# Optimization experiments

Hardware: AMD Instinct MI355X
Metric: run time of the kernel (lower is better)

Reference implementation:

```python
import jax, jax.numpy as jnp
import numpy as np

N_EMB = 256
HEAD_SIZE = 64
B, S = 4, 4096


def setup_inputs() -> dict:
    key = jax.random.key(0)
    k1, k2, k3, k4 = jax.random.split(key, 4)
    return {
        "ini_emb": jax.random.normal(k1, (B, S, N_EMB), dtype=jnp.float32),
        "wk": jax.random.normal(k2, (N_EMB, HEAD_SIZE), dtype=jnp.float32) * (N_EMB ** -0.5),
        "wq": jax.random.normal(k3, (N_EMB, HEAD_SIZE), dtype=jnp.float32) * (N_EMB ** -0.5),
        "wv": jax.random.normal(k4, (N_EMB, HEAD_SIZE), dtype=jnp.float32) * (N_EMB ** -0.5),
    }


def reference(ini_emb, wk, wq, wv):
    # projections: [B,S,E] @ [E,H] -> [B,S,H]
    k = ini_emb @ wk
    q = ini_emb @ wq
    v = ini_emb @ wv
    # scores: [B,S,S]; NOTE: source scales by n_emb**-0.5, not head_size**-0.5
    scores = jnp.einsum("bqh,bkh->bqk", q, k) * (N_EMB ** -0.5)
    attn = jax.nn.softmax(scores, axis=-1)
    # output: [B,S,H]
    return jnp.einsum("bqk,bkh->bqh", attn, v)
```

## Files before the change

### kernel.cpp

```cpp
#include <hip/hip_runtime.h>


typedef short short4v __attribute__((ext_vector_type(4)));
typedef short short8v __attribute__((ext_vector_type(8)));
typedef float floatx4 __attribute__((ext_vector_type(4)));
typedef unsigned short u16;
typedef unsigned int u32;

#define SEQ 4096
#define EMB 256
#define HD 64
#define PADA 264
#define OSTR 68

static __device__ __forceinline__ u16 f2bf(float x) {
    union { float f; unsigned u; } v; v.f = x;
    unsigned r = v.u + 0x7FFFu + ((v.u >> 16) & 1u);
    return (u16)(r >> 16);
}

static __device__ __forceinline__ u32 cvt_pk_bf16(float a, float b) {
    u32 r;
    asm("v_cvt_pk_bf16_f32 %0, %1, %2" : "=v"(r) : "v"(a), "v"(b));
    return r;
}

static __device__ __forceinline__ short4v pack_bf4(float a, float b, float c, float d) {
    union { u32 u[2]; short4v s; } x;
    x.u[0] = cvt_pk_bf16(a, b);
    x.u[1] = cvt_pk_bf16(c, d);
    return x.s;
}

__global__ __launch_bounds__(256) void prep_w(
    const float* __restrict__ wk, const float* __restrict__ wq, const float* __restrict__ wv,
    u16* __restrict__ wt) {
    const int nt = blockIdx.x;
    const int t = threadIdx.x;
#pragma unroll
    for (int ss = 0; ss < 2; ++ss) {
        int slot = t + ss * 256;
        int kc = slot >> 6, lane = slot & 63;
        int ln15 = lane & 15, lq = lane >> 4;
        int cg = nt * 16 + ln15;
        int mat = cg >> 6, col = cg & 63;
        const float* W = (mat == 0) ? wq : (mat == 1) ? wk : wv;
        const float s = (mat == 0) ? 0.0625f * 1.44269504088896f : 1.0f;
        u32 w4[4];
#pragma unroll
        for (int p = 0; p < 2; ++p) {
#pragma unroll
            for (int d = 0; d < 2; ++d) {
                int e0 = kc * 32 + lq * 8 + p * 4 + d * 2;
                u16 lo = f2bf(W[(e0 + 0) * HD + col] * s);
                u16 hi = f2bf(W[(e0 + 1) * HD + col] * s);
                w4[p * 2 + d] = (u32)lo | ((u32)hi << 16);
            }
        }
        u32* dst = (u32*)wt + ((size_t)(nt * 8 + kc) * 64 + lane) * 4;
        *(uint4*)dst = make_uint4(w4[0], w4[1], w4[2], w4[3]);
    }
}

__global__ __launch_bounds__(256) void proj_mfma(
    const float* __restrict__ emb, const u16* __restrict__ wt,
    u16* __restrict__ qb, u16* __restrict__ kb, u16* __restrict__ vbt) {
    __shared__ u16 a_s[16 * PADA];
    const int t = threadIdx.x;
    const int lane = t & 63;
    const int wave = t >> 6;
    const int ln15 = lane & 15;
    const int lq = lane >> 4;
    const size_t row0 = (size_t)blockIdx.x * 16;

#pragma unroll
    for (int c = 0; c < 4; ++c) {
        int f = t + c * 256;
        int row = f >> 6, e4 = (f & 63) * 4;
        float4 v = *(const float4*)(emb + (row0 + row) * EMB + e4);
        u32 lo = cvt_pk_bf16(v.x, v.y);
        u32 hi = cvt_pk_bf16(v.z, v.w);
        *(uint2*)&a_s[row * PADA + e4] = make_uint2(lo, hi);
    }
    __syncthreads();

    floatx4 acc[3];
#pragma unroll
    for (int j = 0; j < 3; ++j) {
        floatx4 z = { 0.f, 0.f, 0.f, 0.f };
        acc[j] = z;
    }

#pragma unroll
    for (int kc = 0; kc < 8; ++kc) {
        short8v a = *(const short8v*)&a_s[ln15 * PADA + kc * 32 + lq * 8];
#pragma unroll
        for (int j = 0; j < 3; ++j) {
            short8v b = *(const short8v*)(wt + (((size_t)(wave * 3 + j) * 8 + kc) * 64 + lane) * 8);
            acc[j] = __builtin_amdgcn_mfma_f32_16x16x32_bf16(a, b, acc[j], 0, 0, 0);
        }
    }

#pragma unroll
    for (int j = 0; j < 3; ++j) {
        int cg = (wave * 3 + j) * 16 + ln15;
        int mat = cg >> 6, col = cg & 63;
        if (mat < 2) {
            u16* O = (mat == 0) ? qb : kb;
#pragma unroll
            for (int r = 0; r < 4; ++r)
                O[(row0 + lq * 4 + r) * HD + col] = f2bf(acc[j][r]);
        } else {
            u32 lo = cvt_pk_bf16(acc[j][0], acc[j][1]);
            u32 hi = cvt_pk_bf16(acc[j][2], acc[j][3]);
            size_t bidx = row0 >> 12;
            size_t sl = (row0 & 4095) + lq * 4;
            *(uint2*)&vbt[(bidx * 64 + col) * SEQ + sl] = make_uint2(lo, hi);
        }
    }
}


template <bool PF>
static __device__ __forceinline__ void attn_step(
    const int tt, const int split, const int wave, const int ln15, const int lq,
    const u16* __restrict__ kpb, const u16* __restrict__ vpb,
    const short8v (&qf)[4][2], const short8v k0c, const short8v k1c,
    short8v& k0n, short8v& k1n,
    floatx4 (&oacc)[4][4], float (&lacc)[4]) {
    const int kw = (split * 16 + tt) * 64 + wave * 16;

    short4v vf[4];
#pragma unroll
    for (int ht = 0; ht < 4; ++ht)
        vf[ht] = *(const short4v*)(vpb + (size_t)(ht * 16 + ln15) * SEQ + kw + lq * 4);

    if (PF) {
        const int kwn = kw + 64;
        k0n = *(const short8v*)(kpb + (size_t)(kwn + ln15) * HD + lq * 8);
        k1n = *(const short8v*)(kpb + (size_t)(kwn + ln15) * HD + 32 + lq * 8);
    }

    floatx4 s[4];
    __builtin_amdgcn_s_setprio(1);
#pragma unroll
    for (int nt = 0; nt < 4; ++nt) {
        floatx4 z = { 0.f, 0.f, 0.f, 0.f };
        s[nt] = __builtin_amdgcn_mfma_f32_16x16x32_bf16(k0c, qf[nt][0], z, 0, 0, 0);
        s[nt] = __builtin_amdgcn_mfma_f32_16x16x32_bf16(k1c, qf[nt][1], s[nt], 0, 0, 0);
    }
    __builtin_amdgcn_s_setprio(0);

    short4v pf[4];
#pragma unroll
    for (int nt = 0; nt < 4; ++nt) {
        float p0 = __builtin_amdgcn_exp2f(s[nt][0]);
        float p1 = __builtin_amdgcn_exp2f(s[nt][1]);
        float p2 = __builtin_amdgcn_exp2f(s[nt][2]);
        float p3 = __builtin_amdgcn_exp2f(s[nt][3]);
        lacc[nt] += (p0 + p1) + (p2 + p3);
        pf[nt] = pack_bf4(p0, p1, p2, p3);
    }

    __builtin_amdgcn_s_setprio(1);
#pragma unroll
    for (int ht = 0; ht < 4; ++ht)
#pragma unroll
        for (int nt = 0; nt < 4; ++nt)
            oacc[ht][nt] = __builtin_amdgcn_mfma_f32_16x16x16bf16_1k(
                vf[ht], pf[nt], oacc[ht][nt], 0, 0, 0);
    __builtin_amdgcn_s_setprio(0);
}

__global__ __launch_bounds__(256) void attn_kernel(
    const u16* __restrict__ qb, const u16* __restrict__ kb, const u16* __restrict__ vbt,
    float* __restrict__ po, float* __restrict__ pml) {
    __shared__ float ored[64 * OSTR];
    __shared__ float lred[4 * 64];

    const int t = threadIdx.x;
    const int lane = t & 63;
    const int wave = t >> 6;
    const int ln15 = lane & 15;
    const int lq = lane >> 4;

    const int part = blockIdx.x;
    const int b = part >> 8;
    const int qt = (part >> 2) & 63;
    const int split = part & 3;
    const int q0 = qt * 64;

    const u16* __restrict__ qpb = qb + ((size_t)b * SEQ + q0) * HD;
    const u16* __restrict__ kpb = kb + (size_t)b * SEQ * HD;
    const u16* __restrict__ vpb = vbt + (size_t)b * HD * SEQ;

    short8v qf[4][2];
#pragma unroll
    for (int nt = 0; nt < 4; ++nt)
#pragma unroll
        for (int h = 0; h < 2; ++h)
            qf[nt][h] = *(const short8v*)(qpb + (size_t)(nt * 16 + ln15) * HD + h * 32 + lq * 8);

    floatx4 oacc[4][4];
#pragma unroll
    for (int ht = 0; ht < 4; ++ht)
#pragma unroll
        for (int nt = 0; nt < 4; ++nt) {
            floatx4 z = { 0.f, 0.f, 0.f, 0.f };
            oacc[ht][nt] = z;
        }
    float lacc[4] = { 0.f, 0.f, 0.f, 0.f };

    short8v kA0, kA1, kB0, kB1;
    {
        const int kw0 = (split * 16) * 64 + wave * 16;
        kA0 = *(const short8v*)(kpb + (size_t)(kw0 + ln15) * HD + lq * 8);
        kA1 = *(const short8v*)(kpb + (size_t)(kw0 + ln15) * HD + 32 + lq * 8);
    }

#pragma unroll 1
    for (int tth = 0; tth < 8; ++tth) {
        attn_step<true>(2 * tth,     split, wave, ln15, lq, kpb, vpb, qf,
                        kA0, kA1, kB0, kB1, oacc, lacc);
        attn_step<true>(2 * tth + 1, split, wave, ln15, lq, kpb, vpb, qf,
                        kB0, kB1, kA0, kA1, oacc, lacc);
    }

#pragma unroll
    for (int nt = 0; nt < 4; ++nt) {
        lacc[nt] += __shfl_xor(lacc[nt], 16);
        lacc[nt] += __shfl_xor(lacc[nt], 32);
    }
    if (lq == 0) {
#pragma unroll
        for (int nt = 0; nt < 4; ++nt)
            lred[wave * 64 + nt * 16 + ln15] = lacc[nt];
    }

    for (int s4 = 0; s4 < 4; ++s4) {
        if (wave == s4) {
#pragma unroll
            for (int nt = 0; nt < 4; ++nt)
#pragma unroll
                for (int ht = 0; ht < 4; ++ht) {
                    int idx = (nt * 16 + ln15) * OSTR + ht * 16 + lq * 4;
                    if (s4 == 0) {
                        *(floatx4*)&ored[idx] = oacc[ht][nt];
                    } else {
                        floatx4 old = *(floatx4*)&ored[idx];
                        old += oacc[ht][nt];
                        *(floatx4*)&ored[idx] = old;
                    }
                }
        }
        __syncthreads();
    }

    float* __restrict__ pob = po + (size_t)part * 4096;
#pragma unroll
    for (int i = 0; i < 4; ++i) {
        int f4 = t + i * 256;
        int q = f4 >> 4, h4 = (f4 & 15) * 4;
        *(float4*)&pob[q * HD + h4] = *(float4*)&ored[q * OSTR + h4];
    }
    if (t < 64)
        pml[part * 64 + t] = lred[t] + lred[64 + t] + lred[128 + t] + lred[192 + t];
}

__global__ __launch_bounds__(256) void reduce_kernel(
    const float* __restrict__ po, const float* __restrict__ pml,
    float* __restrict__ out) {
    __shared__ float ls[64];
    const int t = threadIdx.x;
    const int part0 = blockIdx.x * 4;
    const int bq = blockIdx.x;

    if (t < 64)
        ls[t] = pml[(part0 + 0) * 64 + t] + pml[(part0 + 1) * 64 + t]
              + pml[(part0 + 2) * 64 + t] + pml[(part0 + 3) * 64 + t];
    __syncthreads();

    const float* __restrict__ p0 = po + (size_t)(part0 + 0) * 4096;
    const float* __restrict__ p1 = po + (size_t)(part0 + 1) * 4096;
    const float* __restrict__ p2 = po + (size_t)(part0 + 2) * 4096;
    const float* __restrict__ p3 = po + (size_t)(part0 + 3) * 4096;
    float* __restrict__ ob = out + (((size_t)(bq >> 6) * SEQ + (size_t)(bq & 63) * 64)) * HD;

#pragma unroll
    for (int i = 0; i < 4; ++i) {
        int f4 = t + i * 256;
        int f = f4 * 4;
        int q = f4 >> 4;
        float4 a = *(const float4*)&p0[f];
        float4 c = *(const float4*)&p1[f];
        float4 d = *(const float4*)&p2[f];
        float4 e = *(const float4*)&p3[f];
        float inv = 1.0f / ls[q];
        float4 r;
        r.x = (a.x + c.x + d.x + e.x) * inv;
        r.y = (a.y + c.y + d.y + e.y) * inv;
        r.z = (a.z + c.z + d.z + e.z) * inv;
        r.w = (a.w + c.w + d.w + e.w) * inv;
        *(float4*)&ob[f] = r;
    }
}

extern "C" void kernel_launch(void* const* d_in, const int* in_sizes, int n_in,
                              void* d_out, int out_size, void* d_ws, size_t ws_size,
                              hipStream_t stream) {
    const float* emb = (const float*)d_in[0];
    const float* wk  = (const float*)d_in[1];
    const float* wq  = (const float*)d_in[2];
    const float* wv  = (const float*)d_in[3];

    u16* qb  = (u16*)d_ws;
    u16* kb  = (u16*)((char*)d_ws + (size_t)2 * 1024 * 1024);
    u16* vbt = (u16*)((char*)d_ws + (size_t)4 * 1024 * 1024);
    u16* wt  = (u16*)((char*)d_ws + (size_t)6 * 1024 * 1024);
    float* po  = (float*)((char*)d_ws + (size_t)6 * 1024 * 1024 + 256 * 1024);
    float* pml = (float*)((char*)d_ws + (size_t)22 * 1024 * 1024 + 256 * 1024);
    float* out = (float*)d_out;

    prep_w<<<12, 256, 0, stream>>>(wk, wq, wv, wt);
    proj_mfma<<<1024, 256, 0, stream>>>(emb, wt, qb, kb, vbt);
    attn_kernel<<<1024, 256, 0, stream>>>(qb, kb, vbt, po, pml);
    reduce_kernel<<<256, 256, 0, stream>>>(po, pml, out);
}
```

Before: 136.4 us.

## Halve KV splits, prefetch V fragments, and swizzle block-to-part mapping

Cuts the key-split count from 4 to 2, so each attention block walks 32 key tiles instead of 16, and the grid shrinks to 512 blocks. V fragments are now double-buffered and prefetched one step ahead, like K, with the last step peeled so it skips the prefetch. Block indices are remapped with a stride-8 swizzle, likely to spread work across XCDs and L2. The reduce kernel sums two partials instead of four, which cuts partial-output traffic, at the cost of fewer blocks and less parallelism on a large GPU.

Measured after the change: 131.4 us. 1.04x faster.

```diff
diff --git a/kernel.cpp b/kernel.cpp
--- a/kernel.cpp
+++ b/kernel.cpp
@@ -125,18 +125,17 @@
 static __device__ __forceinline__ void attn_step(
     const int tt, const int split, const int wave, const int ln15, const int lq,
     const u16* __restrict__ kpb, const u16* __restrict__ vpb,
-    const short8v (&qf)[4][2], const short8v k0c, const short8v k1c,
-    short8v& k0n, short8v& k1n,
+    const short8v (&qf)[4][2],
+    const short8v k0c, const short8v k1c, const short4v (&vfc)[4],
+    short8v& k0n, short8v& k1n, short4v (&vfn)[4],
     floatx4 (&oacc)[4][4], float (&lacc)[4]) {
-    const int kw = (split * 16 + tt) * 64 + wave * 16;
-
-    short4v vf[4];
-#pragma unroll
-    for (int ht = 0; ht < 4; ++ht)
-        vf[ht] = *(const short4v*)(vpb + (size_t)(ht * 16 + ln15) * SEQ + kw + lq * 4);
+    const int kw = (split * 32 + tt) * 64 + wave * 16;
 
     if (PF) {
         const int kwn = kw + 64;
+#pragma unroll
+        for (int ht = 0; ht < 4; ++ht)
+            vfn[ht] = *(const short4v*)(vpb + (size_t)(ht * 16 + ln15) * SEQ + kwn + lq * 4);
         k0n = *(const short8v*)(kpb + (size_t)(kwn + ln15) * HD + lq * 8);
         k1n = *(const short8v*)(kpb + (size_t)(kwn + ln15) * HD + 32 + lq * 8);
     }
@@ -168,7 +167,7 @@
 #pragma unroll
         for (int nt = 0; nt < 4; ++nt)
             oacc[ht][nt] = __builtin_amdgcn_mfma_f32_16x16x16bf16_1k(
-                vf[ht], pf[nt], oacc[ht][nt], 0, 0, 0);
+                vfc[ht], pf[nt], oacc[ht][nt], 0, 0, 0);
     __builtin_amdgcn_s_setprio(0);
 }
 
@@ -184,10 +183,10 @@
     const int ln15 = lane & 15;
     const int lq = lane >> 4;
 
-    const int part = blockIdx.x;
-    const int b = part >> 8;
-    const int qt = (part >> 2) & 63;
-    const int split = part & 3;
+    const int part = ((blockIdx.x & 7) << 6) | (blockIdx.x >> 3);
+    const int b = part >> 7;
+    const int qt = (part >> 1) & 63;
+    const int split = part & 1;
     const int q0 = qt * 64;
 
     const u16* __restrict__ qpb = qb + ((size_t)b * SEQ + q0) * HD;
@@ -212,19 +211,27 @@
     float lacc[4] = { 0.f, 0.f, 0.f, 0.f };
 
     short8v kA0, kA1, kB0, kB1;
+    short4v vfA[4], vfB[4];
     {
-        const int kw0 = (split * 16) * 64 + wave * 16;
+        const int kw0 = (split * 32) * 64 + wave * 16;
         kA0 = *(const short8v*)(kpb + (size_t)(kw0 + ln15) * HD + lq * 8);
         kA1 = *(const short8v*)(kpb + (size_t)(kw0 + ln15) * HD + 32 + lq * 8);
+#pragma unroll
+        for (int ht = 0; ht < 4; ++ht)
+            vfA[ht] = *(const short4v*)(vpb + (size_t)(ht * 16 + ln15) * SEQ + kw0 + lq * 4);
     }
 
 #pragma unroll 1
-    for (int tth = 0; tth < 8; ++tth) {
+    for (int tth = 0; tth < 15; ++tth) {
         attn_step<true>(2 * tth,     split, wave, ln15, lq, kpb, vpb, qf,
-                        kA0, kA1, kB0, kB1, oacc, lacc);
+                        kA0, kA1, vfA, kB0, kB1, vfB, oacc, lacc);
         attn_step<true>(2 * tth + 1, split, wave, ln15, lq, kpb, vpb, qf,
-                        kB0, kB1, kA0, kA1, oacc, lacc);
-    }
+                        kB0, kB1, vfB, kA0, kA1, vfA, oacc, lacc);
+    }
+    attn_step<true >(30, split, wave, ln15, lq, kpb, vpb, qf,
+                     kA0, kA1, vfA, kB0, kB1, vfB, oacc, lacc);
+    attn_step<false>(31, split, wave, ln15, lq, kpb, vpb, qf,
+                     kB0, kB1, vfB, kA0, kA1, vfA, oacc, lacc);
 
 #pragma unroll
     for (int nt = 0; nt < 4; ++nt) {
@@ -272,18 +279,15 @@
     float* __restrict__ out) {
     __shared__ float ls[64];
     const int t = threadIdx.x;
-    const int part0 = blockIdx.x * 4;
+    const int part0 = blockIdx.x * 2;
     const int bq = blockIdx.x;
 
     if (t < 64)
-        ls[t] = pml[(part0 + 0) * 64 + t] + pml[(part0 + 1) * 64 + t]
-              + pml[(part0 + 2) * 64 + t] + pml[(part0 + 3) * 64 + t];
+        ls[t] = pml[(part0 + 0) * 64 + t] + pml[(part0 + 1) * 64 + t];
     __syncthreads();
 
     const float* __restrict__ p0 = po + (size_t)(part0 + 0) * 4096;
     const float* __restrict__ p1 = po + (size_t)(part0 + 1) * 4096;
-    const float* __restrict__ p2 = po + (size_t)(part0 + 2) * 4096;
-    const float* __restrict__ p3 = po + (size_t)(part0 + 3) * 4096;
     float* __restrict__ ob = out + (((size_t)(bq >> 6) * SEQ + (size_t)(bq & 63) * 64)) * HD;
 
 #pragma unroll
@@ -293,14 +297,12 @@
         int q = f4 >> 4;
         float4 a = *(const float4*)&p0[f];
         float4 c = *(const float4*)&p1[f];
-        float4 d = *(const float4*)&p2[f];
-        float4 e = *(const float4*)&p3[f];
         float inv = 1.0f / ls[q];
         float4 r;
-        r.x = (a.x + c.x + d.x + e.x) * inv;
-        r.y = (a.y + c.y + d.y + e.y) * inv;
-        r.z = (a.z + c.z + d.z + e.z) * inv;
-        r.w = (a.w + c.w + d.w + e.w) * inv;
+        r.x = (a.x + c.x) * inv;
+        r.y = (a.y + c.y) * inv;
+        r.z = (a.z + c.z) * inv;
+        r.w = (a.w + c.w) * inv;
         *(float4*)&ob[f] = r;
     }
 }
@@ -323,6 +325,6 @@
 
     prep_w<<<12, 256, 0, stream>>>(wk, wq, wv, wt);
     proj_mfma<<<1024, 256, 0, stream>>>(emb, wt, qb, kb, vbt);
-    attn_kernel<<<1024, 256, 0, stream>>>(qb, kb, vbt, po, pml);
+    attn_kernel<<<512, 256, 0, stream>>>(qb, kb, vbt, po, pml);
     reduce_kernel<<<256, 256, 0, stream>>>(po, pml, out);
 }
```

## Stage K/V tiles through swizzled LDS with double buffering; widen projection tiles

Applied to the files above, without the earlier changes.

Attention now loads each 64-key K and V tile cooperatively with coalesced 16-byte global loads into XOR-swizzled, double-buffered shared memory, prefetching the next tile into registers while computing the current one. Before, each wave fetched its own strided fragments straight from global memory. Blocks are also remapped so consecutive block IDs spread across batch and query tiles. Separately, the projection kernel handles 32 rows per block so each weight fragment is reused for two MFMAs. This adds barriers and LDS traffic per tile and halves the number of projection blocks.

New measurement: 119.5 us. 12.4% less time.

```diff
diff --git a/kernel.cpp b/kernel.cpp
--- a/kernel.cpp
+++ b/kernel.cpp
@@ -65,16 +65,16 @@
 __global__ __launch_bounds__(256) void proj_mfma(
     const float* __restrict__ emb, const u16* __restrict__ wt,
     u16* __restrict__ qb, u16* __restrict__ kb, u16* __restrict__ vbt) {
-    __shared__ u16 a_s[16 * PADA];
+    __shared__ u16 a_s[32 * PADA];
     const int t = threadIdx.x;
     const int lane = t & 63;
     const int wave = t >> 6;
     const int ln15 = lane & 15;
     const int lq = lane >> 4;
-    const size_t row0 = (size_t)blockIdx.x * 16;
-
-#pragma unroll
-    for (int c = 0; c < 4; ++c) {
+    const size_t row0 = (size_t)blockIdx.x * 32;
+
+#pragma unroll
+    for (int c = 0; c < 8; ++c) {
         int f = t + c * 256;
         int row = f >> 6, e4 = (f & 63) * 4;
         float4 v = *(const float4*)(emb + (row0 + row) * EMB + e4);
@@ -84,70 +84,73 @@
     }
     __syncthreads();
 
-    floatx4 acc[3];
-#pragma unroll
-    for (int j = 0; j < 3; ++j) {
-        floatx4 z = { 0.f, 0.f, 0.f, 0.f };
-        acc[j] = z;
-    }
+    floatx4 acc[2][3];
+#pragma unroll
+    for (int rg = 0; rg < 2; ++rg)
+#pragma unroll
+        for (int j = 0; j < 3; ++j) {
+            floatx4 z = { 0.f, 0.f, 0.f, 0.f };
+            acc[rg][j] = z;
+        }
 
 #pragma unroll
     for (int kc = 0; kc < 8; ++kc) {
-        short8v a = *(const short8v*)&a_s[ln15 * PADA + kc * 32 + lq * 8];
+        short8v a0 = *(const short8v*)&a_s[ln15 * PADA + kc * 32 + lq * 8];
+        short8v a1 = *(const short8v*)&a_s[(16 + ln15) * PADA + kc * 32 + lq * 8];
 #pragma unroll
         for (int j = 0; j < 3; ++j) {
             short8v b = *(const short8v*)(wt + (((size_t)(wave * 3 + j) * 8 + kc) * 64 + lane) * 8);
-            acc[j] = __builtin_amdgcn_mfma_f32_16x16x32_bf16(a, b, acc[j], 0, 0, 0);
-        }
-    }
-
-#pragma unroll
-    for (int j = 0; j < 3; ++j) {
-        int cg = (wave * 3 + j) * 16 + ln15;
-        int mat = cg >> 6, col = cg & 63;
-        if (mat < 2) {
-            u16* O = (mat == 0) ? qb : kb;
-#pragma unroll
-            for (int r = 0; r < 4; ++r)
-                O[(row0 + lq * 4 + r) * HD + col] = f2bf(acc[j][r]);
-        } else {
-            u32 lo = cvt_pk_bf16(acc[j][0], acc[j][1]);
-            u32 hi = cvt_pk_bf16(acc[j][2], acc[j][3]);
-            size_t bidx = row0 >> 12;
-            size_t sl = (row0 & 4095) + lq * 4;
-            *(uint2*)&vbt[(bidx * 64 + col) * SEQ + sl] = make_uint2(lo, hi);
-        }
-    }
-}
-
-
-template <bool PF>
-static __device__ __forceinline__ void attn_step(
-    const int tt, const int split, const int wave, const int ln15, const int lq,
-    const u16* __restrict__ kpb, const u16* __restrict__ vpb,
-    const short8v (&qf)[4][2], const short8v k0c, const short8v k1c,
-    short8v& k0n, short8v& k1n,
-    floatx4 (&oacc)[4][4], float (&lacc)[4]) {
-    const int kw = (split * 16 + tt) * 64 + wave * 16;
-
+            acc[0][j] = __builtin_amdgcn_mfma_f32_16x16x32_bf16(a0, b, acc[0][j], 0, 0, 0);
+            acc[1][j] = __builtin_amdgcn_mfma_f32_16x16x32_bf16(a1, b, acc[1][j], 0, 0, 0);
+        }
+    }
+
+#pragma unroll
+    for (int rg = 0; rg < 2; ++rg) {
+        const size_t row0g = row0 + rg * 16;
+#pragma unroll
+        for (int j = 0; j < 3; ++j) {
+            int cg = (wave * 3 + j) * 16 + ln15;
+            int mat = cg >> 6, col = cg & 63;
+            if (mat < 2) {
+                u16* O = (mat == 0) ? qb : kb;
+#pragma unroll
+                for (int r = 0; r < 4; ++r)
+                    O[(row0g + lq * 4 + r) * HD + col] = f2bf(acc[rg][j][r]);
+            } else {
+                u32 lo = cvt_pk_bf16(acc[rg][j][0], acc[rg][j][1]);
+                u32 hi = cvt_pk_bf16(acc[rg][j][2], acc[rg][j][3]);
+                size_t bidx = row0g >> 12;
+                size_t sl = (row0g & 4095) + lq * 4;
+                *(uint2*)&vbt[(bidx * 64 + col) * SEQ + sl] = make_uint2(lo, hi);
+            }
+        }
+    }
+}
+
+
+struct AttnCtx {
+    int ksw_lo, ksw_hi, voff, ln15, lq;
+};
+
+static __device__ __forceinline__ void attn_compute(
+    const u16* __restrict__ kt, const u16* __restrict__ vt, const AttnCtx& cx,
+    const short8v (&qf)[4][2], floatx4 (&oacc)[4][4], float (&lacc)[4]) {
     short4v vf[4];
 #pragma unroll
     for (int ht = 0; ht < 4; ++ht)
-        vf[ht] = *(const short4v*)(vpb + (size_t)(ht * 16 + ln15) * SEQ + kw + lq * 4);
-
-    if (PF) {
-        const int kwn = kw + 64;
-        k0n = *(const short8v*)(kpb + (size_t)(kwn + ln15) * HD + lq * 8);
-        k1n = *(const short8v*)(kpb + (size_t)(kwn + ln15) * HD + 32 + lq * 8);
-    }
+        vf[ht] = *(const short4v*)(vt + (ht * 16 + cx.ln15) * 64 + cx.voff);
+
+    short8v k0 = *(const short8v*)(kt + cx.ksw_lo);
+    short8v k1 = *(const short8v*)(kt + cx.ksw_hi);
 
     floatx4 s[4];
     __builtin_amdgcn_s_setprio(1);
 #pragma unroll
     for (int nt = 0; nt < 4; ++nt) {
         floatx4 z = { 0.f, 0.f, 0.f, 0.f };
-        s[nt] = __builtin_amdgcn_mfma_f32_16x16x32_bf16(k0c, qf[nt][0], z, 0, 0, 0);
-        s[nt] = __builtin_amdgcn_mfma_f32_16x16x32_bf16(k1c, qf[nt][1], s[nt], 0, 0, 0);
+        s[nt] = __builtin_amdgcn_mfma_f32_16x16x32_bf16(k0, qf[nt][0], z, 0, 0, 0);
+        s[nt] = __builtin_amdgcn_mfma_f32_16x16x32_bf16(k1, qf[nt][1], s[nt], 0, 0, 0);
     }
     __builtin_amdgcn_s_setprio(0);
 
@@ -175,7 +178,7 @@
 __global__ __launch_bounds__(256) void attn_kernel(
     const u16* __restrict__ qb, const u16* __restrict__ kb, const u16* __restrict__ vbt,
     float* __restrict__ po, float* __restrict__ pml) {
-    __shared__ float ored[64 * OSTR];
+    __shared__ __align__(16) u16 smem[4][64 * 64];
     __shared__ float lred[4 * 64];
 
     const int t = threadIdx.x;
@@ -184,7 +187,7 @@
     const int ln15 = lane & 15;
     const int lq = lane >> 4;
 
-    const int part = blockIdx.x;
+    const int part = ((blockIdx.x & 7) << 7) | (blockIdx.x >> 3);
     const int b = part >> 8;
     const int qt = (part >> 2) & 63;
     const int split = part & 3;
@@ -211,20 +214,53 @@
         }
     float lacc[4] = { 0.f, 0.f, 0.f, 0.f };
 
-    short8v kA0, kA1, kB0, kB1;
-    {
-        const int kw0 = (split * 16) * 64 + wave * 16;
-        kA0 = *(const short8v*)(kpb + (size_t)(kw0 + ln15) * HD + lq * 8);
-        kA1 = *(const short8v*)(kpb + (size_t)(kw0 + ln15) * HD + 32 + lq * 8);
-    }
+    const int r0 = t >> 3, c0 = t & 7;
+    const int r1 = (t + 256) >> 3;
+    const int sw0 = r0 * 64 + ((c0 ^ (r0 & 7)) * 8);
+    const int sw1 = r1 * 64 + ((c0 ^ (r1 & 7)) * 8);
+
+    AttnCtx cx;
+    cx.ln15 = ln15; cx.lq = lq;
+    const int krow = wave * 16 + ln15;
+    cx.ksw_lo = krow * 64 + (((0 + lq) ^ (ln15 & 7)) * 8);
+    cx.ksw_hi = krow * 64 + (((4 + lq) ^ (ln15 & 7)) * 8);
+    const int vch = wave * 2 + (lq >> 1);
+    cx.voff = ((vch ^ (ln15 & 7)) * 8) + (lq & 1) * 4;
+
+    uint4 kraA, krbA, vraA, vrbA;
+    uint4 kraB, krbB, vraB, vrbB;
+
+#define LOADT(n, KA, KB, VA, VB) { const int kwb = (split * 16 + (n)) * 64;            \
+        KA = *(const uint4*)(kpb + (size_t)(kwb + r0) * HD + c0 * 8);                  \
+        KB = *(const uint4*)(kpb + (size_t)(kwb + r1) * HD + c0 * 8);                  \
+        VA = *(const uint4*)(vpb + (size_t)r0 * SEQ + kwb + c0 * 8);                   \
+        VB = *(const uint4*)(vpb + (size_t)r1 * SEQ + kwb + c0 * 8); }
+#define WRITET(B, KA, KB, VA, VB) { u16* kt_ = &smem[(B) * 2][0]; u16* vt_ = &smem[(B) * 2 + 1][0]; \
+        *(uint4*)(kt_ + sw0) = KA; *(uint4*)(kt_ + sw1) = KB;                          \
+        *(uint4*)(vt_ + sw0) = VA; *(uint4*)(vt_ + sw1) = VB; }
+
+    LOADT(0, kraA, krbA, vraA, vrbA);
+    LOADT(1, kraB, krbB, vraB, vrbB);
+    WRITET(0, kraA, krbA, vraA, vrbA);
+    __syncthreads();
 
 #pragma unroll 1
-    for (int tth = 0; tth < 8; ++tth) {
-        attn_step<true>(2 * tth,     split, wave, ln15, lq, kpb, vpb, qf,
-                        kA0, kA1, kB0, kB1, oacc, lacc);
-        attn_step<true>(2 * tth + 1, split, wave, ln15, lq, kpb, vpb, qf,
-                        kB0, kB1, kA0, kA1, oacc, lacc);
-    }
+    for (int th = 0; th < 8; ++th) {
+        if (th < 7) LOADT(2 * th + 2, kraA, krbA, vraA, vrbA);
+        attn_compute(&smem[0][0], &smem[1][0], cx, qf, oacc, lacc);
+        WRITET(1, kraB, krbB, vraB, vrbB);
+        __syncthreads();
+        if (th < 7) {
+            LOADT(2 * th + 3, kraB, krbB, vraB, vrbB);
+        }
+        attn_compute(&smem[2][0], &smem[3][0], cx, qf, oacc, lacc);
+        if (th < 7) {
+            WRITET(0, kraA, krbA, vraA, vrbA);
+        }
+        __syncthreads();
+    }
+#undef LOADT
+#undef WRITET
 
 #pragma unroll
     for (int nt = 0; nt < 4; ++nt) {
@@ -237,6 +273,7 @@
             lred[wave * 64 + nt * 16 + ln15] = lacc[nt];
     }
 
+    float* ored = (float*)&smem[0][0];
     for (int s4 = 0; s4 < 4; ++s4) {
         if (wave == s4) {
 #pragma unroll
@@ -322,7 +359,7 @@
     float* out = (float*)d_out;
 
     prep_w<<<12, 256, 0, stream>>>(wk, wq, wv, wt);
-    proj_mfma<<<1024, 256, 0, stream>>>(emb, wt, qb, kb, vbt);
+    proj_mfma<<<512, 256, 0, stream>>>(emb, wt, qb, kb, vbt);
     attn_kernel<<<1024, 256, 0, stream>>>(qb, kb, vbt, po, pml);
     reduce_kernel<<<256, 256, 0, stream>>>(po, pml, out);
 }
```
